# Performance work log

Hardware: AMD Instinct MI355X
Metric: run time of the kernel (lower is better)

Reference implementation:

```python
import jax, jax.numpy as jnp
import numpy as np

D_MODEL = 1024
D_STATE = 16
D_CONV = 4
D_INNER = 2 * D_MODEL  # expand=2
DT_RANK = D_MODEL // D_STATE  # ceil(1024/16) = 64


def setup_inputs() -> dict:
    key = jax.random.key(0)
    ks = jax.random.split(key, 8)
    rn = lambda k, shape, s: jax.random.normal(k, shape, jnp.float32) * s
    return {
        "x": jax.random.normal(ks[0], (4, 50, 10240), jnp.float32),
        "in_proj_w": rn(ks[1], (2 * D_INNER, D_MODEL), 0.02),
        "conv_w": rn(ks[2], (D_INNER, D_CONV), 0.2),
        "conv_b": jnp.zeros((D_INNER,), jnp.float32),
        "x_proj_w": rn(ks[3], (DT_RANK + 2 * D_STATE, D_INNER), 0.02),
        "dt_proj_w": rn(ks[4], (D_INNER, DT_RANK), 0.1),
        "dt_proj_b": jnp.log(jnp.expm1(jnp.full((D_INNER,), 0.01, jnp.float32))),
        "A_log": jnp.log(jnp.tile(jnp.arange(1, D_STATE + 1, dtype=jnp.float32), (D_INNER, 1))),
        "D": jnp.ones((D_INNER,), jnp.float32),
        "out_proj_w": rn(ks[5], (D_MODEL, D_INNER), 0.02),
        "fc1_w": rn(ks[6], (D_MODEL, 10240), 0.01),
        "fc1_b": jnp.zeros((D_MODEL,), jnp.float32),
    }


def _mamba(x, in_proj_w, conv_w, conv_b, x_proj_w, dt_proj_w, dt_proj_b, A_log, Dp, out_proj_w):
    # x: (B, L, d_model)
    B, L, _ = x.shape
    xz = x @ in_proj_w.T                          # (B, L, 2*d_inner)
    xi, z = jnp.split(xz, 2, axis=-1)             # (B, L, d_inner) each
    # causal depthwise conv1d along L
    xc = jnp.transpose(xi, (0, 2, 1))             # (B, d_inner, L)
    kern = conv_w[:, None, :]                     # (d_inner, 1, K)
    xc = jax.lax.conv_general_dilated(
        xc, kern, window_strides=(1,), padding=[(D_CONV - 1, 0)],
        dimension_numbers=("NCH", "OIH", "NCH"), feature_group_count=D_INNER)
    xc = jax.nn.silu(jnp.transpose(xc, (0, 2, 1)) + conv_b)  # (B, L, d_inner)
    # input-dependent SSM parameters
    x_dbl = xc @ x_proj_w.T                       # (B, L, dt_rank + 2*N)
    dt, Bm, Cm = jnp.split(x_dbl, [DT_RANK, DT_RANK + D_STATE], axis=-1)
    delta = jax.nn.softplus(dt @ dt_proj_w.T + dt_proj_b)    # (B, L, d_inner)
    A = -jnp.exp(A_log)                           # (d_inner, N)
    dA = jnp.exp(delta[..., None] * A)            # (B, L, d_inner, N)
    dBu = delta[..., None] * Bm[:, :, None, :] * xc[..., None]

    def step(h, ab):
        a, b = ab
        h = a * h + b
        return h, h

    h0 = jnp.zeros((B, D_INNER, D_STATE), x.dtype)
    hs = jax.lax.scan(step, h0, (jnp.swapaxes(dA, 0, 1), jnp.swapaxes(dBu, 0, 1)))[1]  # (L, B, d_inner, N)
    y = jnp.einsum("lbdn,bln->bld", hs, Cm) + xc * Dp       # (B, L, d_inner)
    y = y * jax.nn.silu(z)
    return y @ out_proj_w.T                       # (B, L, d_model)


def reference(x, in_proj_w, conv_w, conv_b, x_proj_w, dt_proj_w, dt_proj_b, A_log, D, out_proj_w, fc1_w, fc1_b):
    b, c, l = x.shape
    xm = x.reshape(b, c * 10, l // 10)            # (b, c*10, 1024)
    xm = _mamba(xm, in_proj_w, conv_w, conv_b, x_proj_w, dt_proj_w, dt_proj_b, A_log, D, out_proj_w)
    xm = xm.reshape(b, c, l)                      # (b, c, 10240)
    # dropout is identity in eval mode
    return jnp.tanh(xm @ fc1_w.T + fc1_b)         # (b, c, 1024)
```

## Files before the change

### kernel.cpp

```cpp
#include <hip/hip_runtime.h>
#include <math.h>

#define BDIM 256

constexpr int B_  = 4;
constexpr int L_  = 500;
constexpr int DM  = 1024;
constexpr int DI  = 2048;
constexpr int DXZ = 4096;
constexpr int RNK = 64;
constexpr int NST = 16;
constexpr int NXP = 96;
constexpr int M1  = B_ * L_;
constexpr int M2  = 200;
constexpr int K2  = 10240;
constexpr int NC  = 20;
constexpr int LC  = L_ / NC;

typedef __attribute__((ext_vector_type(8))) __bf16 bf16x8;
typedef __attribute__((ext_vector_type(4))) __bf16 bf16x4;
typedef __attribute__((ext_vector_type(4))) float  f32x4;

__device__ __forceinline__ float sigmoidf_(float x) { return 1.0f / (1.0f + __expf(-x)); }

__global__ __launch_bounds__(BDIM)
void split_w_k(const float* __restrict__ W, __bf16* __restrict__ Wh,
               __bf16* __restrict__ Wl, int n4)
{
    int i = blockIdx.x * BDIM + threadIdx.x;
    if (i >= n4) return;
    float4 v = *(const float4*)(W + (size_t)i * 4);
    float vv[4] = {v.x, v.y, v.z, v.w};
    bf16x4 hv, lv;
    #pragma unroll
    for (int j = 0; j < 4; ++j) {
        __bf16 h = (__bf16)vv[j];
        hv[j] = h;
        lv[j] = (__bf16)(vv[j] - (float)h);
    }
    *(bf16x4*)(Wh + (size_t)i * 4) = hv;
    *(bf16x4*)(Wl + (size_t)i * 4) = lv;
}

template<int TR>
__device__ __forceinline__ void load_tile(const float* __restrict__ G, int ldg, int valid,
                                          float4* rg, int tid)
{
    #pragma unroll
    for (int i = 0; i < TR / 32; ++i) {
        int f = tid + i * 256;
        int r = f >> 3;
        int c = (f & 7) << 2;
        float4 v = make_float4(0.f, 0.f, 0.f, 0.f);
        if (r < valid) v = *(const float4*)(G + (size_t)r * ldg + c);
        rg[i] = v;
    }
}

template<int TR>
__device__ __forceinline__ void write_tile(const float4* rg, __bf16 (*H)[40], __bf16 (*Lo)[40], int tid)
{
    #pragma unroll
    for (int i = 0; i < TR / 32; ++i) {
        int f = tid + i * 256;
        int r = f >> 3;
        int c = (f & 7) << 2;
        float vv[4] = {rg[i].x, rg[i].y, rg[i].z, rg[i].w};
        bf16x4 hv, lv;
        #pragma unroll
        for (int j = 0; j < 4; ++j) {
            __bf16 h = (__bf16)vv[j];
            hv[j] = h;
            lv[j] = (__bf16)(vv[j] - (float)h);
        }
        *(bf16x4*)&H[r][c]  = hv;
        *(bf16x4*)&Lo[r][c] = lv;
    }
}

template<int TR>
__device__ __forceinline__ void load_wtile(const __bf16* __restrict__ Wh, const __bf16* __restrict__ Wl,
                                           int ldb, int valid, bf16x8* rh, bf16x8* rl, int tid)
{
    #pragma unroll
    for (int i = 0; i < TR / 64; ++i) {
        int f = tid + i * 256;
        int r = f >> 2;
        int c = (f & 3) * 8;
        bf16x8 hv = {}, lv = {};
        if (r < valid) {
            hv = *(const bf16x8*)(Wh + (size_t)r * ldb + c);
            lv = *(const bf16x8*)(Wl + (size_t)r * ldb + c);
        }
        rh[i] = hv;
        rl[i] = lv;
    }
}

template<int TR>
__device__ __forceinline__ void store_wtile(const bf16x8* rh, const bf16x8* rl,
                                            __bf16 (*H)[40], __bf16 (*Lo)[40], int tid)
{
    #pragma unroll
    for (int i = 0; i < TR / 64; ++i) {
        int f = tid + i * 256;
        int r = f >> 2;
        int c = (f & 3) * 8;
        *(bf16x8*)&H[r][c]  = rh[i];
        *(bf16x8*)&Lo[r][c] = rl[i];
    }
}

template<int BM, int BN, int FM, int FN, int FUSE>
__global__ __launch_bounds__(256)
void gemm_pw(const float* __restrict__ A, int lda,
             const __bf16* __restrict__ Bwh, const __bf16* __restrict__ Bwl, int ldb,
             float* __restrict__ C, int ldc,
             int M, int N, int Kchunk, long csplit_stride,
             const float* __restrict__ bias)
{
    __shared__ __bf16 Ah[BM][40], Al[BM][40], Bh[BN][40], Bl[BN][40];
    const int tid  = threadIdx.x;
    const int lane = tid & 63;
    const int wave = tid >> 6;
    const int wm = wave >> 1, wn = wave & 1;
    const int m0 = blockIdx.y * BM;
    const int n0 = blockIdx.x * BN;
    const long kbase = (long)blockIdx.z * Kchunk;
    const float*  Ap  = A   + (size_t)m0 * lda + kbase;
    const __bf16* Bph = Bwh + (size_t)n0 * ldb + kbase;
    const __bf16* Bpl = Bwl + (size_t)n0 * ldb + kbase;
    const int validA = min(BM, M - m0);
    const int validB = min(BN, N - n0);
    f32x4 acc[FM][FN] = {};
    const int fr = lane & 15;
    const int kq = (lane >> 4) * 8;

    float4 ra[BM / 32];
    bf16x8 rbh[BN / 64], rbl[BN / 64];
    load_tile<BM>(Ap, lda, validA, ra, tid);
    load_wtile<BN>(Bph, Bpl, ldb, validB, rbh, rbl, tid);

    for (int k0 = 0; k0 < Kchunk; k0 += 32) {
        write_tile<BM>(ra, Ah, Al, tid);
        store_wtile<BN>(rbh, rbl, Bh, Bl, tid);
        __syncthreads();
        if (k0 + 32 < Kchunk) {
            load_tile<BM>(Ap + k0 + 32, lda, validA, ra, tid);
            load_wtile<BN>(Bph + k0 + 32, Bpl + k0 + 32, ldb, validB, rbh, rbl, tid);
        }
        bf16x8 ah[FM], al[FM], bh[FN], bl[FN];
        #pragma unroll
        for (int i = 0; i < FM; ++i) {
            int r = wm * (FM * 16) + i * 16 + fr;
            ah[i] = *(const bf16x8*)&Ah[r][kq];
            al[i] = *(const bf16x8*)&Al[r][kq];
        }
        #pragma unroll
        for (int j = 0; j < FN; ++j) {
            int r = wn * (FN * 16) + j * 16 + fr;
            bh[j] = *(const bf16x8*)&Bh[r][kq];
            bl[j] = *(const bf16x8*)&Bl[r][kq];
        }
        #pragma unroll
        for (int i = 0; i < FM; ++i)
            #pragma unroll
            for (int j = 0; j < FN; ++j) {
                acc[i][j] = __builtin_amdgcn_mfma_f32_16x16x32_bf16(ah[i], bh[j], acc[i][j], 0, 0, 0);
                acc[i][j] = __builtin_amdgcn_mfma_f32_16x16x32_bf16(ah[i], bl[j], acc[i][j], 0, 0, 0);
                acc[i][j] = __builtin_amdgcn_mfma_f32_16x16x32_bf16(al[i], bh[j], acc[i][j], 0, 0, 0);
            }
        __syncthreads();
    }

    float* Cp = C + (size_t)blockIdx.z * csplit_stride;
    #pragma unroll
    for (int i = 0; i < FM; ++i)
        #pragma unroll
        for (int j = 0; j < FN; ++j)
            #pragma unroll
            for (int r = 0; r < 4; ++r) {
                int gm = m0 + wm * (FM * 16) + i * 16 + (lane >> 4) * 4 + r;
                int gn = n0 + wn * (FN * 16) + j * 16 + (lane & 15);
                if (gm < M && gn < N) {
                    float v = acc[i][j][r];
                    if (FUSE == 1) { v += bias[gn]; v = (v > 20.f) ? v : log1pf(__expf(v)); }
                    Cp[(size_t)gm * ldc + gn] = v;
                }
            }
}

template<int FUSE>
__global__ __launch_bounds__(256)
void reduce_k(const float* __restrict__ part, float* __restrict__ C,
              int MN, int N, int S, long stride, const float* __restrict__ bias)
{
    int i = blockIdx.x * 256 + threadIdx.x;
    if (i >= MN) return;
    float s = 0.f;
    for (int j = 0; j < S; ++j) s += part[(size_t)j * stride + i];
    if (FUSE == 2) s = tanhf(s + bias[i % N]);
    C[i] = s;
}

__global__ __launch_bounds__(BDIM)
void conv_silu_k(const float* __restrict__ xz, const float* __restrict__ cw,
                 const float* __restrict__ cb, float* __restrict__ xc)
{
    int idx = blockIdx.x * BDIM + threadIdx.x;
    if (idx >= M1 * DI) return;
    int d = idx & (DI - 1);
    int m = idx >> 11;
    int b = m / L_, l = m - b * L_;
    float acc = cb[d];
    #pragma unroll
    for (int t = 0; t < 4; ++t) {
        int ls = l - 3 + t;
        if (ls >= 0)
            acc = fmaf(cw[d * 4 + t], xz[(size_t)(b * L_ + ls) * DXZ + d], acc);
    }
    xc[idx] = acc * sigmoidf_(acc);
}

__global__ __launch_bounds__(BDIM)
void scan_partial_k(const float* __restrict__ delta, const float* __restrict__ xc,
                    const float* __restrict__ xdbl, const float* __restrict__ A_log,
                    float* __restrict__ hpart, float* __restrict__ aprod)
{
    const int t = blockIdx.x * BDIM + threadIdx.x;
    const int d = t & (DI - 1);
    const int bc = t >> 11;
    const int b = bc / NC, c = bc - b * NC;
    const int l0 = c * LC;
    float Aa[NST];
    #pragma unroll
    for (int q = 0; q < 4; ++q) {
        float4 a4 = *(const float4*)(A_log + (size_t)d * NST + q * 4);
        Aa[q*4+0] = -__expf(a4.x); Aa[q*4+1] = -__expf(a4.y);
        Aa[q*4+2] = -__expf(a4.z); Aa[q*4+3] = -__expf(a4.w);
    }
    const float* dlt = delta + ((size_t)(b * L_ + l0)) * DI + d;
    const float* xcd = xc    + ((size_t)(b * L_ + l0)) * DI + d;
    const float* bp  = xdbl  + ((size_t)(b * L_ + l0)) * NXP + RNK;
    float h[NST] = {};
    float sdv = 0.f;
    for (int l = 0; l < LC; ++l) {
        float dv = dlt[(size_t)l * DI];
        float xv = xcd[(size_t)l * DI];
        const float4* b4 = (const float4*)(bp + (size_t)l * NXP);
        float dvx = dv * xv;
        sdv += dv;
        #pragma unroll
        for (int q = 0; q < 4; ++q) {
            float4 Bq = b4[q];
            float bb[4] = {Bq.x, Bq.y, Bq.z, Bq.w};
            #pragma unroll
            for (int j = 0; j < 4; ++j) {
                int n = q * 4 + j;
                float dA = __expf(dv * Aa[n]);
                h[n] = fmaf(dA, h[n], dvx * bb[j]);
            }
        }
    }
    float4* hp4 = (float4*)(hpart + (size_t)t * NST);
    float4* ap4 = (float4*)(aprod + (size_t)t * NST);
    #pragma unroll
    for (int q = 0; q < 4; ++q) {
        hp4[q] = make_float4(h[q*4], h[q*4+1], h[q*4+2], h[q*4+3]);
        ap4[q] = make_float4(__expf(Aa[q*4+0]*sdv), __expf(Aa[q*4+1]*sdv),
                             __expf(Aa[q*4+2]*sdv), __expf(Aa[q*4+3]*sdv));
    }
}

__global__ __launch_bounds__(BDIM)
void scan_fix_k(float* __restrict__ hpart, const float* __restrict__ aprod)
{
    const int i = blockIdx.x * BDIM + threadIdx.x;
    if (i >= B_ * DI * NST) return;
    const int nn = i & (NST - 1);
    const int d  = (i >> 4) & (DI - 1);
    const int b  = i >> 15;
    float h = 0.f;
    for (int c = 0; c < NC; ++c) {
        size_t o = ((size_t)((b * NC + c) * DI + d)) * NST + nn;
        float hp = hpart[o];
        float ap = aprod[o];
        hpart[o] = h;
        h = fmaf(ap, h, hp);
    }
}

__global__ __launch_bounds__(BDIM)
void scan_final_k(const float* __restrict__ xz, const float* __restrict__ xc,
                  const float* __restrict__ xdbl, const float* __restrict__ delta,
                  const float* __restrict__ A_log, const float* __restrict__ Dp,
                  const float* __restrict__ hpre, float* __restrict__ y)
{
    const int t = blockIdx.x * BDIM + threadIdx.x;
    const int d = t & (DI - 1);
    const int bc = t >> 11;
    const int b = bc / NC, c = bc - b * NC;
    const int l0 = c * LC;
    float Aa[NST];
    #pragma unroll
    for (int q = 0; q < 4; ++q) {
        float4 a4 = *(const float4*)(A_log + (size_t)d * NST + q * 4);
        Aa[q*4+0] = -__expf(a4.x); Aa[q*4+1] = -__expf(a4.y);
        Aa[q*4+2] = -__expf(a4.z); Aa[q*4+3] = -__expf(a4.w);
    }
    float h[NST];
    const float4* h4 = (const float4*)(hpre + (size_t)t * NST);
    #pragma unroll
    for (int q = 0; q < 4; ++q) {
        float4 hv = h4[q];
        h[q*4+0] = hv.x; h[q*4+1] = hv.y; h[q*4+2] = hv.z; h[q*4+3] = hv.w;
    }
    const float Dd = Dp[d];
    const float* dlt = delta + ((size_t)(b * L_ + l0)) * DI + d;
    const float* xcd = xc    + ((size_t)(b * L_ + l0)) * DI + d;
    const float* bp  = xdbl  + ((size_t)(b * L_ + l0)) * NXP + RNK;
    const float* zp  = xz    + ((size_t)(b * L_ + l0)) * DXZ + DI + d;
    float* yp = y + ((size_t)(b * L_ + l0)) * DI + d;
    for (int l = 0; l < LC; ++l) {
        float dv = dlt[(size_t)l * DI];
        float xv = xcd[(size_t)l * DI];
        const float4* b4 = (const float4*)(bp + (size_t)l * NXP);
        float dvx = dv * xv;
        float p = 0.f;
        #pragma unroll
        for (int q = 0; q < 4; ++q) {
            float4 Bq = b4[q];
            float4 Cq = b4[4 + q];
            float bb[4] = {Bq.x, Bq.y, Bq.z, Bq.w};
            float cc[4] = {Cq.x, Cq.y, Cq.z, Cq.w};
            #pragma unroll
            for (int j = 0; j < 4; ++j) {
                int n = q * 4 + j;
                float dA = __expf(dv * Aa[n]);
                h[n] = fmaf(dA, h[n], dvx * bb[j]);
                p = fmaf(h[n], cc[j], p);
            }
        }
        float zv = zp[(size_t)l * DXZ];
        float yv = fmaf(xv, Dd, p);
        yv *= zv * sigmoidf_(zv);
        yp[(size_t)l * DI] = yv;
    }
}

extern "C" void kernel_launch(void* const* d_in, const int* in_sizes, int n_in,
                              void* d_out, int out_size, void* d_ws, size_t ws_size,
                              hipStream_t stream) {
    const float* x         = (const float*)d_in[0];
    const float* in_proj_w = (const float*)d_in[1];
    const float* conv_w    = (const float*)d_in[2];
    const float* conv_b    = (const float*)d_in[3];
    const float* x_proj_w  = (const float*)d_in[4];
    const float* dt_proj_w = (const float*)d_in[5];
    const float* dt_proj_b = (const float*)d_in[6];
    const float* A_log     = (const float*)d_in[7];
    const float* Dp        = (const float*)d_in[8];
    const float* out_proj_w= (const float*)d_in[9];
    const float* fc1_w     = (const float*)d_in[10];
    const float* fc1_b     = (const float*)d_in[11];
    float* out = (float*)d_out;

    float* ws    = (float*)d_ws;
    float* xz    = ws;
    float* xc    = xz + (size_t)M1 * DXZ;
    float* xdbl  = xc + (size_t)M1 * DI;
    float* delta = xdbl + (size_t)M1 * NXP;
    float* hpart = delta + (size_t)M1 * DI;
    float* aprod = hpart + (size_t)B_ * NC * DI * NST;
    float* y     = delta;
    float* partx = delta;
    float* partO = xz;
    float* ym    = xc;
    float* partf = delta;

    __bf16* W1h = (__bf16*)hpart;
    __bf16* W1l = (__bf16*)aprod;
    __bf16* xph = (__bf16*)hpart;
    __bf16* xpl = xph + (size_t)NXP * DI;
    __bf16* dph = xpl + (size_t)NXP * DI;
    __bf16* dpl = dph + (size_t)DI * RNK;
    __bf16* W4h = (__bf16*)xc;
    __bf16* W4l = W4h + (size_t)DM * DI;
    __bf16* f1h = (__bf16*)xz;
    __bf16* f1l = (__bf16*)hpart;

    dim3 blk(BDIM);
    split_w_k<<<(DXZ*DM/4 + 255)/256, blk, 0, stream>>>(in_proj_w, W1h, W1l, DXZ*DM/4);
    gemm_pw<128,128,4,4,0><<<dim3(DXZ/128, (M1+127)/128, 1), blk, 0, stream>>>(
        x, DM, W1h, W1l, DM, xz, DXZ, M1, DXZ, DM, 0, nullptr);
    conv_silu_k<<<(M1*DI + BDIM-1)/BDIM, blk, 0, stream>>>(xz, conv_w, conv_b, xc);
    split_w_k<<<(NXP*DI/4 + 255)/256, blk, 0, stream>>>(x_proj_w, xph, xpl, NXP*DI/4);
    split_w_k<<<(DI*RNK/4 + 255)/256, blk, 0, stream>>>(dt_proj_w, dph, dpl, DI*RNK/4);
    gemm_pw<64,64,2,2,0><<<dim3((NXP+63)/64, (M1+63)/64, 8), blk, 0, stream>>>(
        xc, DI, xph, xpl, DI, partx, NXP, M1, NXP, DI/8, (long)M1*NXP, nullptr);
    reduce_k<0><<<(M1*NXP + 255)/256, blk, 0, stream>>>(
        partx, xdbl, M1*NXP, NXP, 8, (long)M1*NXP, nullptr);
    gemm_pw<64,64,2,2,1><<<dim3(DI/64, (M1+63)/64, 1), blk, 0, stream>>>(
        xdbl, NXP, dph, dpl, RNK, delta, DI, M1, DI, RNK, 0, dt_proj_b);
    scan_partial_k<<<(B_*NC*DI)/BDIM, blk, 0, stream>>>(
        delta, xc, xdbl, A_log, hpart, aprod);
    scan_fix_k<<<(B_*DI*NST + BDIM-1)/BDIM, blk, 0, stream>>>(hpart, aprod);
    scan_final_k<<<(B_*NC*DI)/BDIM, blk, 0, stream>>>(
        xz, xc, xdbl, delta, A_log, Dp, hpart, y);
    split_w_k<<<(DM*DI/4 + 255)/256, blk, 0, stream>>>(out_proj_w, W4h, W4l, DM*DI/4);
    gemm_pw<64,64,2,2,0><<<dim3(DM/64, (M1+63)/64, 4), blk, 0, stream>>>(
        y, DI, W4h, W4l, DI, partO, DM, M1, DM, DI/4, (long)M1*DM, nullptr);
    reduce_k<0><<<(M1*DM + 255)/256, blk, 0, stream>>>(
        partO, ym, M1*DM, DM, 4, (long)M1*DM, nullptr);
    split_w_k<<<(DM*K2/4 + 255)/256, blk, 0, stream>>>(fc1_w, f1h, f1l, DM*K2/4);
    gemm_pw<64,64,2,2,0><<<dim3(DM/64, (M2+63)/64, 20), blk, 0, stream>>>(
        ym, K2, f1h, f1l, K2, partf, DM, M2, DM, K2/20, (long)M2*DM, nullptr);
    reduce_k<2><<<(M2*DM + 255)/256, blk, 0, stream>>>(
        partf, out, M2*DM, DM, 20, (long)M2*DM, fc1_b);
    (void)in_sizes; (void)n_in; (void)out_size; (void)ws_size;
}
```

Measured before the change: 288.9 us.

## Pre-split activations into bf16 hi/lo planes and stream fc1 weights as fp32

Activations (x, xc, xdbl, y, the out_proj result) are now written as bf16 hi/lo pairs by the producing kernels or by a split pass, so the GEMMs load ready-made bf16 tiles instead of converting fp32 tiles inside the main loop. For the fc1 GEMM the big weight matrix is read as fp32 and split in-kernel, which removes the separate split pass over that 10240x1024 weight and its extra write and read. In exchange there are extra split launches and extra global writes for the activation planes, and the workspace is re-aliased, which risks buffers overlapping one another.

```diff
diff --git a/kernel.cpp b/kernel.cpp
--- a/kernel.cpp
+++ b/kernel.cpp
@@ -24,8 +24,8 @@
 __device__ __forceinline__ float sigmoidf_(float x) { return 1.0f / (1.0f + __expf(-x)); }
 
 __global__ __launch_bounds__(BDIM)
-void split_w_k(const float* __restrict__ W, __bf16* __restrict__ Wh,
-               __bf16* __restrict__ Wl, int n4)
+void split_hl_k(const float* __restrict__ W, __bf16* __restrict__ Wh,
+                __bf16* __restrict__ Wl, int n4)
 {
     int i = blockIdx.x * BDIM + threadIdx.x;
     if (i >= n4) return;
@@ -43,8 +43,41 @@
 }
 
 template<int TR>
-__device__ __forceinline__ void load_tile(const float* __restrict__ G, int ldg, int valid,
-                                          float4* rg, int tid)
+__device__ __forceinline__ void load_hl(const __bf16* __restrict__ Gh, const __bf16* __restrict__ Gl,
+                                        int ldg, int valid, bf16x8* rh, bf16x8* rl, int tid)
+{
+    #pragma unroll
+    for (int i = 0; i < TR / 64; ++i) {
+        int f = tid + i * 256;
+        int r = f >> 2;
+        int c = (f & 3) * 8;
+        bf16x8 hv = {}, lv = {};
+        if (r < valid) {
+            hv = *(const bf16x8*)(Gh + (size_t)r * ldg + c);
+            lv = *(const bf16x8*)(Gl + (size_t)r * ldg + c);
+        }
+        rh[i] = hv;
+        rl[i] = lv;
+    }
+}
+
+template<int TR>
+__device__ __forceinline__ void store_hl(const bf16x8* rh, const bf16x8* rl,
+                                         __bf16 (*H)[40], __bf16 (*Lo)[40], int tid)
+{
+    #pragma unroll
+    for (int i = 0; i < TR / 64; ++i) {
+        int f = tid + i * 256;
+        int r = f >> 2;
+        int c = (f & 3) * 8;
+        *(bf16x8*)&H[r][c]  = rh[i];
+        *(bf16x8*)&Lo[r][c] = rl[i];
+    }
+}
+
+template<int TR>
+__device__ __forceinline__ void load_f32(const float* __restrict__ G, int ldg, int valid,
+                                         float4* rg, int tid)
 {
     #pragma unroll
     for (int i = 0; i < TR / 32; ++i) {
@@ -58,7 +91,7 @@
 }
 
 template<int TR>
-__device__ __forceinline__ void write_tile(const float4* rg, __bf16 (*H)[40], __bf16 (*Lo)[40], int tid)
+__device__ __forceinline__ void store_f32split(const float4* rg, __bf16 (*H)[40], __bf16 (*Lo)[40], int tid)
 {
     #pragma unroll
     for (int i = 0; i < TR / 32; ++i) {
@@ -78,102 +111,41 @@
     }
 }
 
-template<int TR>
-__device__ __forceinline__ void load_wtile(const __bf16* __restrict__ Wh, const __bf16* __restrict__ Wl,
-                                           int ldb, int valid, bf16x8* rh, bf16x8* rl, int tid)
-{
-    #pragma unroll
-    for (int i = 0; i < TR / 64; ++i) {
-        int f = tid + i * 256;
-        int r = f >> 2;
-        int c = (f & 3) * 8;
-        bf16x8 hv = {}, lv = {};
-        if (r < valid) {
-            hv = *(const bf16x8*)(Wh + (size_t)r * ldb + c);
-            lv = *(const bf16x8*)(Wl + (size_t)r * ldb + c);
-        }
-        rh[i] = hv;
-        rl[i] = lv;
-    }
-}
-
-template<int TR>
-__device__ __forceinline__ void store_wtile(const bf16x8* rh, const bf16x8* rl,
-                                            __bf16 (*H)[40], __bf16 (*Lo)[40], int tid)
-{
-    #pragma unroll
-    for (int i = 0; i < TR / 64; ++i) {
-        int f = tid + i * 256;
-        int r = f >> 2;
-        int c = (f & 3) * 8;
-        *(bf16x8*)&H[r][c]  = rh[i];
-        *(bf16x8*)&Lo[r][c] = rl[i];
-    }
-}
-
-template<int BM, int BN, int FM, int FN, int FUSE>
-__global__ __launch_bounds__(256)
-void gemm_pw(const float* __restrict__ A, int lda,
-             const __bf16* __restrict__ Bwh, const __bf16* __restrict__ Bwl, int ldb,
-             float* __restrict__ C, int ldc,
-             int M, int N, int Kchunk, long csplit_stride,
-             const float* __restrict__ bias)
-{
-    __shared__ __bf16 Ah[BM][40], Al[BM][40], Bh[BN][40], Bl[BN][40];
-    const int tid  = threadIdx.x;
-    const int lane = tid & 63;
-    const int wave = tid >> 6;
-    const int wm = wave >> 1, wn = wave & 1;
-    const int m0 = blockIdx.y * BM;
-    const int n0 = blockIdx.x * BN;
-    const long kbase = (long)blockIdx.z * Kchunk;
-    const float*  Ap  = A   + (size_t)m0 * lda + kbase;
-    const __bf16* Bph = Bwh + (size_t)n0 * ldb + kbase;
-    const __bf16* Bpl = Bwl + (size_t)n0 * ldb + kbase;
-    const int validA = min(BM, M - m0);
-    const int validB = min(BN, N - n0);
-    f32x4 acc[FM][FN] = {};
+template<int BM, int BN, int FM, int FN>
+__device__ __forceinline__ void mfma_step(__bf16 (*Ah)[40], __bf16 (*Al)[40],
+                                          __bf16 (*Bh)[40], __bf16 (*Bl)[40],
+                                          f32x4 (&acc)[FM][FN], int wm, int wn, int lane)
+{
     const int fr = lane & 15;
     const int kq = (lane >> 4) * 8;
-
-    float4 ra[BM / 32];
-    bf16x8 rbh[BN / 64], rbl[BN / 64];
-    load_tile<BM>(Ap, lda, validA, ra, tid);
-    load_wtile<BN>(Bph, Bpl, ldb, validB, rbh, rbl, tid);
-
-    for (int k0 = 0; k0 < Kchunk; k0 += 32) {
-        write_tile<BM>(ra, Ah, Al, tid);
-        store_wtile<BN>(rbh, rbl, Bh, Bl, tid);
-        __syncthreads();
-        if (k0 + 32 < Kchunk) {
-            load_tile<BM>(Ap + k0 + 32, lda, validA, ra, tid);
-            load_wtile<BN>(Bph + k0 + 32, Bpl + k0 + 32, ldb, validB, rbh, rbl, tid);
-        }
-        bf16x8 ah[FM], al[FM], bh[FN], bl[FN];
-        #pragma unroll
-        for (int i = 0; i < FM; ++i) {
-            int r = wm * (FM * 16) + i * 16 + fr;
-            ah[i] = *(const bf16x8*)&Ah[r][kq];
-            al[i] = *(const bf16x8*)&Al[r][kq];
-        }
+    bf16x8 ah[FM], al[FM], bh[FN], bl[FN];
+    #pragma unroll
+    for (int i = 0; i < FM; ++i) {
+        int r = wm * (FM * 16) + i * 16 + fr;
+        ah[i] = *(const bf16x8*)&Ah[r][kq];
+        al[i] = *(const bf16x8*)&Al[r][kq];
+    }
+    #pragma unroll
+    for (int j = 0; j < FN; ++j) {
+        int r = wn * (FN * 16) + j * 16 + fr;
+        bh[j] = *(const bf16x8*)&Bh[r][kq];
+        bl[j] = *(const bf16x8*)&Bl[r][kq];
+    }
+    #pragma unroll
+    for (int i = 0; i < FM; ++i)
         #pragma unroll
         for (int j = 0; j < FN; ++j) {
-            int r = wn * (FN * 16) + j * 16 + fr;
-            bh[j] = *(const bf16x8*)&Bh[r][kq];
-            bl[j] = *(const bf16x8*)&Bl[r][kq];
-        }
-        #pragma unroll
-        for (int i = 0; i < FM; ++i)
-            #pragma unroll
-            for (int j = 0; j < FN; ++j) {
-                acc[i][j] = __builtin_amdgcn_mfma_f32_16x16x32_bf16(ah[i], bh[j], acc[i][j], 0, 0, 0);
-                acc[i][j] = __builtin_amdgcn_mfma_f32_16x16x32_bf16(ah[i], bl[j], acc[i][j], 0, 0, 0);
-                acc[i][j] = __builtin_amdgcn_mfma_f32_16x16x32_bf16(al[i], bh[j], acc[i][j], 0, 0, 0);
-            }
-        __syncthreads();
-    }
-
-    float* Cp = C + (size_t)blockIdx.z * csplit_stride;
+            acc[i][j] = __builtin_amdgcn_mfma_f32_16x16x32_bf16(ah[i], bh[j], acc[i][j], 0, 0, 0);
+            acc[i][j] = __builtin_amdgcn_mfma_f32_16x16x32_bf16(ah[i], bl[j], acc[i][j], 0, 0, 0);
+            acc[i][j] = __builtin_amdgcn_mfma_f32_16x16x32_bf16(al[i], bh[j], acc[i][j], 0, 0, 0);
+        }
+}
+
+template<int BM, int BN, int FM, int FN, int FUSE>
+__device__ __forceinline__ void epilogue(f32x4 (&acc)[FM][FN], float* __restrict__ C, int ldc,
+                                         int m0, int n0, int M, int N, int wm, int wn, int lane,
+                                         const float* __restrict__ bias)
+{
     #pragma unroll
     for (int i = 0; i < FM; ++i)
         #pragma unroll
@@ -185,27 +157,128 @@
                 if (gm < M && gn < N) {
                     float v = acc[i][j][r];
                     if (FUSE == 1) { v += bias[gn]; v = (v > 20.f) ? v : log1pf(__expf(v)); }
-                    Cp[(size_t)gm * ldc + gn] = v;
+                    C[(size_t)gm * ldc + gn] = v;
                 }
             }
 }
 
-template<int FUSE>
+template<int BM, int BN, int FM, int FN, int FUSE>
 __global__ __launch_bounds__(256)
-void reduce_k(const float* __restrict__ part, float* __restrict__ C,
-              int MN, int N, int S, long stride, const float* __restrict__ bias)
+void gemm_bb(const __bf16* __restrict__ Agh, const __bf16* __restrict__ Agl, int lda,
+             const __bf16* __restrict__ Bgh, const __bf16* __restrict__ Bgl, int ldb,
+             float* __restrict__ C, int ldc,
+             int M, int N, int Kchunk, long csplit_stride,
+             const float* __restrict__ bias)
+{
+    __shared__ __bf16 Ah[BM][40], Al[BM][40], Bh[BN][40], Bl[BN][40];
+    const int tid  = threadIdx.x;
+    const int lane = tid & 63;
+    const int wave = tid >> 6;
+    const int wm = wave >> 1, wn = wave & 1;
+    const int m0 = blockIdx.y * BM;
+    const int n0 = blockIdx.x * BN;
+    const long kbase = (long)blockIdx.z * Kchunk;
+    const __bf16* Aph = Agh + (size_t)m0 * lda + kbase;
+    const __bf16* Apl = Agl + (size_t)m0 * lda + kbase;
+    const __bf16* Bph = Bgh + (size_t)n0 * ldb + kbase;
+    const __bf16* Bpl = Bgl + (size_t)n0 * ldb + kbase;
+    const int validA = min(BM, M - m0);
+    const int validB = min(BN, N - n0);
+    f32x4 acc[FM][FN] = {};
+
+    bf16x8 rah[BM / 64], ral[BM / 64], rbh[BN / 64], rbl[BN / 64];
+    load_hl<BM>(Aph, Apl, lda, validA, rah, ral, tid);
+    load_hl<BN>(Bph, Bpl, ldb, validB, rbh, rbl, tid);
+
+    for (int k0 = 0; k0 < Kchunk; k0 += 32) {
+        store_hl<BM>(rah, ral, Ah, Al, tid);
+        store_hl<BN>(rbh, rbl, Bh, Bl, tid);
+        __syncthreads();
+        if (k0 + 32 < Kchunk) {
+            load_hl<BM>(Aph + k0 + 32, Apl + k0 + 32, lda, validA, rah, ral, tid);
+            load_hl<BN>(Bph + k0 + 32, Bpl + k0 + 32, ldb, validB, rbh, rbl, tid);
+        }
+        mfma_step<BM, BN, FM, FN>(Ah, Al, Bh, Bl, acc, wm, wn, lane);
+        __syncthreads();
+    }
+    epilogue<BM, BN, FM, FN, FUSE>(acc, C + (size_t)blockIdx.z * csplit_stride, ldc,
+                                   m0, n0, M, N, wm, wn, lane, bias);
+}
+
+template<int BM, int BN, int FM, int FN, int FUSE>
+__global__ __launch_bounds__(256)
+void gemm_ab(const __bf16* __restrict__ Agh, const __bf16* __restrict__ Agl, int lda,
+             const float* __restrict__ Bw, int ldb,
+             float* __restrict__ C, int ldc,
+             int M, int N, int Kchunk, long csplit_stride,
+             const float* __restrict__ bias)
+{
+    __shared__ __bf16 Ah[BM][40], Al[BM][40], Bh[BN][40], Bl[BN][40];
+    const int tid  = threadIdx.x;
+    const int lane = tid & 63;
+    const int wave = tid >> 6;
+    const int wm = wave >> 1, wn = wave & 1;
+    const int m0 = blockIdx.y * BM;
+    const int n0 = blockIdx.x * BN;
+    const long kbase = (long)blockIdx.z * Kchunk;
+    const __bf16* Aph = Agh + (size_t)m0 * lda + kbase;
+    const __bf16* Apl = Agl + (size_t)m0 * lda + kbase;
+    const float* Bp = Bw + (size_t)n0 * ldb + kbase;
+    const int validA = min(BM, M - m0);
+    const int validB = min(BN, N - n0);
+    f32x4 acc[FM][FN] = {};
+
+    bf16x8 rah[BM / 64], ral[BM / 64];
+    float4 rb[BN / 32];
+    load_hl<BM>(Aph, Apl, lda, validA, rah, ral, tid);
+    load_f32<BN>(Bp, ldb, validB, rb, tid);
+
+    for (int k0 = 0; k0 < Kchunk; k0 += 32) {
+        store_hl<BM>(rah, ral, Ah, Al, tid);
+        store_f32split<BN>(rb, Bh, Bl, tid);
+        __syncthreads();
+        if (k0 + 32 < Kchunk) {
+            load_hl<BM>(Aph + k0 + 32, Apl + k0 + 32, lda, validA, rah, ral, tid);
+            load_f32<BN>(Bp + k0 + 32, ldb, validB, rb, tid);
+        }
+        mfma_step<BM, BN, FM, FN>(Ah, Al, Bh, Bl, acc, wm, wn, lane);
+        __syncthreads();
+    }
+    epilogue<BM, BN, FM, FN, FUSE>(acc, C + (size_t)blockIdx.z * csplit_stride, ldc,
+                                   m0, n0, M, N, wm, wn, lane, bias);
+}
+
+template<bool F32OUT>
+__global__ __launch_bounds__(256)
+void reduce_hl_k(const float* __restrict__ part, float* __restrict__ C,
+                 __bf16* __restrict__ Ch, __bf16* __restrict__ Cl,
+                 int MN, int S, long stride)
 {
     int i = blockIdx.x * 256 + threadIdx.x;
     if (i >= MN) return;
     float s = 0.f;
     for (int j = 0; j < S; ++j) s += part[(size_t)j * stride + i];
-    if (FUSE == 2) s = tanhf(s + bias[i % N]);
-    C[i] = s;
+    if (F32OUT) C[i] = s;
+    __bf16 h = (__bf16)s;
+    Ch[i] = h;
+    Cl[i] = (__bf16)(s - (float)h);
+}
+
+__global__ __launch_bounds__(256)
+void reduce_tanh_k(const float* __restrict__ part, float* __restrict__ C,
+                   int MN, int N, int S, long stride, const float* __restrict__ bias)
+{
+    int i = blockIdx.x * 256 + threadIdx.x;
+    if (i >= MN) return;
+    float s = 0.f;
+    for (int j = 0; j < S; ++j) s += part[(size_t)j * stride + i];
+    C[i] = tanhf(s + bias[i % N]);
 }
 
 __global__ __launch_bounds__(BDIM)
-void conv_silu_k(const float* __restrict__ xz, const float* __restrict__ cw,
-                 const float* __restrict__ cb, float* __restrict__ xc)
+void conv_silu_hl_k(const float* __restrict__ xz, const float* __restrict__ cw,
+                    const float* __restrict__ cb, float* __restrict__ xc,
+                    __bf16* __restrict__ xch, __bf16* __restrict__ xcl)
 {
     int idx = blockIdx.x * BDIM + threadIdx.x;
     if (idx >= M1 * DI) return;
@@ -219,7 +292,11 @@
         if (ls >= 0)
             acc = fmaf(cw[d * 4 + t], xz[(size_t)(b * L_ + ls) * DXZ + d], acc);
     }
-    xc[idx] = acc * sigmoidf_(acc);
+    float r = acc * sigmoidf_(acc);
+    xc[idx] = r;
+    __bf16 h = (__bf16)r;
+    xch[idx] = h;
+    xcl[idx] = (__bf16)(r - (float)h);
 }
 
 __global__ __launch_bounds__(BDIM)
@@ -375,47 +452,57 @@
     float* y     = delta;
     float* partx = delta;
     float* partO = xz;
-    float* ym    = xc;
     float* partf = delta;
-
+    float* ym    = nullptr;
+
+    __bf16* xh  = (__bf16*)xc;
+    __bf16* xl  = xh + (size_t)M1 * DM;
     __bf16* W1h = (__bf16*)hpart;
     __bf16* W1l = (__bf16*)aprod;
-    __bf16* xph = (__bf16*)hpart;
+    __bf16* hb  = (__bf16*)hpart;
+    __bf16* xph = hb;
     __bf16* xpl = xph + (size_t)NXP * DI;
     __bf16* dph = xpl + (size_t)NXP * DI;
     __bf16* dpl = dph + (size_t)DI * RNK;
-    __bf16* W4h = (__bf16*)xc;
+    __bf16* xch = dpl + (size_t)DI * RNK;
+    __bf16* xcl = xch + (size_t)M1 * DI;
+    __bf16* xdh = xcl + (size_t)M1 * DI;
+    __bf16* xdl = xdh + (size_t)M1 * NXP;
+    __bf16* yh  = (__bf16*)xc;
+    __bf16* yl  = yh + (size_t)M1 * DI;
+    __bf16* W4h = (__bf16*)hpart;
     __bf16* W4l = W4h + (size_t)DM * DI;
-    __bf16* f1h = (__bf16*)xz;
-    __bf16* f1l = (__bf16*)hpart;
+    __bf16* ymh = (__bf16*)aprod;
+    __bf16* yml = ymh + (size_t)M1 * DM;
 
     dim3 blk(BDIM);
-    split_w_k<<<(DXZ*DM/4 + 255)/256, blk, 0, stream>>>(in_proj_w, W1h, W1l, DXZ*DM/4);
-    gemm_pw<128,128,4,4,0><<<dim3(DXZ/128, (M1+127)/128, 1), blk, 0, stream>>>(
-        x, DM, W1h, W1l, DM, xz, DXZ, M1, DXZ, DM, 0, nullptr);
-    conv_silu_k<<<(M1*DI + BDIM-1)/BDIM, blk, 0, stream>>>(xz, conv_w, conv_b, xc);
-    split_w_k<<<(NXP*DI/4 + 255)/256, blk, 0, stream>>>(x_proj_w, xph, xpl, NXP*DI/4);
-    split_w_k<<<(DI*RNK/4 + 255)/256, blk, 0, stream>>>(dt_proj_w, dph, dpl, DI*RNK/4);
-    gemm_pw<64,64,2,2,0><<<dim3((NXP+63)/64, (M1+63)/64, 8), blk, 0, stream>>>(
-        xc, DI, xph, xpl, DI, partx, NXP, M1, NXP, DI/8, (long)M1*NXP, nullptr);
-    reduce_k<0><<<(M1*NXP + 255)/256, blk, 0, stream>>>(
-        partx, xdbl, M1*NXP, NXP, 8, (long)M1*NXP, nullptr);
-    gemm_pw<64,64,2,2,1><<<dim3(DI/64, (M1+63)/64, 1), blk, 0, stream>>>(
-        xdbl, NXP, dph, dpl, RNK, delta, DI, M1, DI, RNK, 0, dt_proj_b);
+    split_hl_k<<<(M1*DM/4 + 255)/256, blk, 0, stream>>>(x, xh, xl, M1*DM/4);
+    split_hl_k<<<(DXZ*DM/4 + 255)/256, blk, 0, stream>>>(in_proj_w, W1h, W1l, DXZ*DM/4);
+    gemm_bb<128,128,4,4,0><<<dim3(DXZ/128, (M1+127)/128, 1), blk, 0, stream>>>(
+        xh, xl, DM, W1h, W1l, DM, xz, DXZ, M1, DXZ, DM, 0, nullptr);
+    conv_silu_hl_k<<<(M1*DI + BDIM-1)/BDIM, blk, 0, stream>>>(xz, conv_w, conv_b, xc, xch, xcl);
+    split_hl_k<<<(NXP*DI/4 + 255)/256, blk, 0, stream>>>(x_proj_w, xph, xpl, NXP*DI/4);
+    split_hl_k<<<(DI*RNK/4 + 255)/256, blk, 0, stream>>>(dt_proj_w, dph, dpl, DI*RNK/4);
+    gemm_bb<64,64,2,2,0><<<dim3((NXP+63)/64, (M1+63)/64, 8), blk, 0, stream>>>(
+        xch, xcl, DI, xph, xpl, DI, partx, NXP, M1, NXP, DI/8, (long)M1*NXP, nullptr);
+    reduce_hl_k<true><<<(M1*NXP + 255)/256, blk, 0, stream>>>(
+        partx, xdbl, xdh, xdl, M1*NXP, 8, (long)M1*NXP);
+    gemm_bb<64,64,2,2,1><<<dim3(DI/64, (M1+63)/64, 1), blk, 0, stream>>>(
+        xdh, xdl, NXP, dph, dpl, RNK, delta, DI, M1, DI, RNK, 0, dt_proj_b);
     scan_partial_k<<<(B_*NC*DI)/BDIM, blk, 0, stream>>>(
         delta, xc, xdbl, A_log, hpart, aprod);
     scan_fix_k<<<(B_*DI*NST + BDIM-1)/BDIM, blk, 0, stream>>>(hpart, aprod);
     scan_final_k<<<(B_*NC*DI)/BDIM, blk, 0, stream>>>(
         xz, xc, xdbl, delta, A_log, Dp, hpart, y);
-    split_w_k<<<(DM*DI/4 + 255)/256, blk, 0, stream>>>(out_proj_w, W4h, W4l, DM*DI/4);
-    gemm_pw<64,64,2,2,0><<<dim3(DM/64, (M1+63)/64, 4), blk, 0, stream>>>(
-        y, DI, W4h, W4l, DI, partO, DM, M1, DM, DI/4, (long)M1*DM, nullptr);
-    reduce_k<0><<<(M1*DM + 255)/256, blk, 0, stream>>>(
-        partO, ym, M1*DM, DM, 4, (long)M1*DM, nullptr);
-    split_w_k<<<(DM*K2/4 + 255)/256, blk, 0, stream>>>(fc1_w, f1h, f1l, DM*K2/4);
-    gemm_pw<64,64,2,2,0><<<dim3(DM/64, (M2+63)/64, 20), blk, 0, stream>>>(
-        ym, K2, f1h, f1l, K2, partf, DM, M2, DM, K2/20, (long)M2*DM, nullptr);
-    reduce_k<2><<<(M2*DM + 255)/256, blk, 0, stream>>>(
+    split_hl_k<<<(M1*DI/4 + 255)/256, blk, 0, stream>>>(y, yh, yl, M1*DI/4);
+    split_hl_k<<<(DM*DI/4 + 255)/256, blk, 0, stream>>>(out_proj_w, W4h, W4l, DM*DI/4);
+    gemm_bb<64,64,2,2,0><<<dim3(DM/64, (M1+63)/64, 4), blk, 0, stream>>>(
+        yh, yl, DI, W4h, W4l, DI, partO, DM, M1, DM, DI/4, (long)M1*DM, nullptr);
+    reduce_hl_k<false><<<(M1*DM + 255)/256, blk, 0, stream>>>(
+        partO, nullptr, ymh, yml, M1*DM, 4, (long)M1*DM);
+    gemm_ab<64,64,2,2,0><<<dim3(DM/64, (M2+63)/64, 20), blk, 0, stream>>>(
+        ymh, yml, K2, fc1_w, K2, partf, DM, M2, DM, K2/20, (long)M2*DM, nullptr);
+    reduce_tanh_k<<<(M2*DM + 255)/256, blk, 0, stream>>>(
         partf, out, M2*DM, DM, 20, (long)M2*DM, fc1_b);
-    (void)in_sizes; (void)n_in; (void)out_size; (void)ws_size;
-}
+    (void)in_sizes; (void)n_in; (void)out_size; (void)ws_size; (void)ym;
+}
```

After: 294.4 us. Within noise of the previous version (+1.9%).
